# Kernel optimization log

Measured on AMD Instinct MI355X. Metric: run time of the kernel, lower is better.

Reference implementation:

```python
import jax, jax.numpy as jnp
import numpy as np

B, S, D, H, DFF = 4, 2048, 2048, 16, 8192
DH = D // H
THETA = 10000.0
EPS = 1e-5


def rmsnorm(x, g):
    return x * jax.lax.rsqrt(jnp.mean(x * x, axis=-1, keepdims=True) + EPS) * g


def rope(x, pos):
    # x: [B, H, S, DH]; rotate interleaved even/odd pairs
    half = DH // 2
    inv_freq = THETA ** (-(jnp.arange(half, dtype=jnp.float32) * 2.0) / DH)  # [half]
    ang = pos.astype(jnp.float32)[:, None] * inv_freq  # [S, half]
    cos, sin = jnp.cos(ang), jnp.sin(ang)
    x1, x2 = x[..., 0::2], x[..., 1::2]
    r1 = x1 * cos - x2 * sin
    r2 = x1 * sin + x2 * cos
    return jnp.stack([r1, r2], axis=-1).reshape(x.shape)


def setup_inputs() -> dict:
    key = jax.random.key(0)
    ks = jax.random.split(key, 12)
    s = 0.02
    return {
        "x": jax.random.normal(ks[0], (B, S, D), dtype=jnp.float32),
        "attention_mask": jnp.ones((S, S), dtype=bool),
        "wq": jax.random.normal(ks[1], (D, D), dtype=jnp.float32) * s,
        "wk": jax.random.normal(ks[2], (D, D), dtype=jnp.float32) * s,
        "wv": jax.random.normal(ks[3], (D, D), dtype=jnp.float32) * s,
        "wo": jax.random.normal(ks[4], (D, D), dtype=jnp.float32) * s,
        "w1": jax.random.normal(ks[5], (DFF, D), dtype=jnp.float32) * s,
        "w2": jax.random.normal(ks[6], (D, DFF), dtype=jnp.float32) * s,
        "w3": jax.random.normal(ks[7], (DFF, D), dtype=jnp.float32) * s,
        "g1": jnp.ones((D,), dtype=jnp.float32),
        "g2": jnp.ones((D,), dtype=jnp.float32),
    }


def reference(x, attention_mask, wq, wk, wv, wo, w1, w2, w3, g1, g2):
    pos = jnp.arange(x.shape[-2])
    # pre-norm attention
    h = rmsnorm(x, g1)
    q = (h @ wq.T).reshape(B, S, H, DH).transpose(0, 2, 1, 3)
    k = (h @ wk.T).reshape(B, S, H, DH).transpose(0, 2, 1, 3)
    v = (h @ wv.T).reshape(B, S, H, DH).transpose(0, 2, 1, 3)
    q = rope(q, pos)
    k = rope(k, pos)
    scores = jnp.einsum("bhqd,bhkd->bhqk", q, k) / np.float32(np.sqrt(DH))
    scores = jnp.where(attention_mask, scores, jnp.float32(-1e9))
    attn = jax.nn.softmax(scores, axis=-1)
    o = jnp.einsum("bhqk,bhkd->bhqd", attn, v)
    o = o.transpose(0, 2, 1, 3).reshape(B, S, D) @ wo.T
    x = x + o
    # pre-norm SwiGLU FFN
    h2 = rmsnorm(x, g2)
    ffn = (jax.nn.silu(h2 @ w1.T) * (h2 @ w3.T)) @ w2.T
    return x + ffn
```

## Files before the change

### kernel.cpp

```cpp
#include <hip/hip_runtime.h>
#include <cstdint>
#include <cstddef>

#define B_   4
#define S_   2048
#define D_   2048
#define H_   16
#define DH_  128
#define DFF_ 8192
#define LOG2E 1.4426950408889634f

typedef __bf16 bf16_t;
typedef __bf16 bf16x4 __attribute__((ext_vector_type(4)));
typedef __bf16 bf16x8 __attribute__((ext_vector_type(8)));
typedef float  f32x4  __attribute__((ext_vector_type(4)));

#define MFMA16 __builtin_amdgcn_mfma_f32_16x16x32_bf16

__device__ __forceinline__ void glds16(const void* g, void* l) {
  __builtin_amdgcn_global_load_lds((__attribute__((address_space(1))) void*)g,
                                   (__attribute__((address_space(3))) void*)l,
                                   16, 0, 0);
}

__global__ __launch_bounds__(256) void cvt_kernel(const float* __restrict__ in,
                                                  bf16_t* __restrict__ out, int n8) {
  int i = blockIdx.x * 256 + threadIdx.x;
  if (i >= n8) return;
  const float4* p4 = (const float4*)in;
  float4 a = p4[2 * (size_t)i];
  float4 b = p4[2 * (size_t)i + 1];
  bf16x8 o;
  o[0] = (bf16_t)a.x; o[1] = (bf16_t)a.y; o[2] = (bf16_t)a.z; o[3] = (bf16_t)a.w;
  o[4] = (bf16_t)b.x; o[5] = (bf16_t)b.y; o[6] = (bf16_t)b.z; o[7] = (bf16_t)b.w;
  ((bf16x8*)out)[i] = o;
}

__global__ __launch_bounds__(256) void rmsnorm_kernel(const float* __restrict__ x,
                                                      const float* __restrict__ g,
                                                      bf16_t* __restrict__ out) {
  const int row = blockIdx.x, tid = threadIdx.x;
  const float* xr = x + (size_t)row * D_;
  float4 a = ((const float4*)xr)[tid * 2];
  float4 b = ((const float4*)xr)[tid * 2 + 1];
  float ss = a.x*a.x + a.y*a.y + a.z*a.z + a.w*a.w
           + b.x*b.x + b.y*b.y + b.z*b.z + b.w*b.w;
#pragma unroll
  for (int m = 1; m < 64; m <<= 1) ss += __shfl_xor(ss, m);
  __shared__ float red[4];
  if ((tid & 63) == 0) red[tid >> 6] = ss;
  __syncthreads();
  float tot = red[0] + red[1] + red[2] + red[3];
  float rms = rsqrtf(tot * (1.0f / D_) + 1e-5f);
  float4 ga = ((const float4*)g)[tid * 2];
  float4 gb = ((const float4*)g)[tid * 2 + 1];
  bf16x8 o;
  o[0] = (bf16_t)(a.x * rms * ga.x); o[1] = (bf16_t)(a.y * rms * ga.y);
  o[2] = (bf16_t)(a.z * rms * ga.z); o[3] = (bf16_t)(a.w * rms * ga.w);
  o[4] = (bf16_t)(b.x * rms * gb.x); o[5] = (bf16_t)(b.y * rms * gb.y);
  o[6] = (bf16_t)(b.z * rms * gb.z); o[7] = (bf16_t)(b.w * rms * gb.w);
  ((bf16x8*)out)[(size_t)row * 256 + tid] = o;
}


#define Q_RD_A(d, mg)                                                         \
  do {                                                                        \
    const char* p_ = ldsb + (d) * 32768 + (wm * 128 + (mg) * 64 + l15) * 128; \
    _Pragma("unroll") for (int i_ = 0; i_ < 4; i_++) {                        \
      afr[i_][0] = *(const bf16x8*)(p_ + i_ * 2048 + acol0);                  \
      afr[i_][1] = *(const bf16x8*)(p_ + i_ * 2048 + acol1);                  \
    }                                                                         \
  } while (0)

#define Q_RD_B(dst, d, ng)                                                    \
  do {                                                                        \
    const char* p_ = ldsb + 65536 + (d) * 32768 +                             \
                     (wn * 64 + (ng) * 32 + l15) * 128;                       \
    _Pragma("unroll") for (int j_ = 0; j_ < 2; j_++) {                        \
      dst[j_][0] = *(const bf16x8*)(p_ + j_ * 2048 + acol0);                  \
      dst[j_][1] = *(const bf16x8*)(p_ + j_ * 2048 + acol1);                  \
    }                                                                         \
  } while (0)

#define Q_STAGE_A(d, kt)                                                      \
  do {                                                                        \
    char* dst_ = ldsb + (d) * 32768 + o0;                                     \
    const bf16_t* s_ = Asrc + (size_t)(kt) * 64;                              \
    glds16(s_, dst_);                                                         \
    glds16(s_ + 64 * (size_t)K, dst_ + 8192);                                 \
    glds16(s_ + 128 * (size_t)K, dst_ + 16384);                               \
    glds16(s_ + 192 * (size_t)K, dst_ + 24576);                               \
  } while (0)

#define Q_STAGE_B(d, kt)                                                      \
  do {                                                                        \
    char* dst_ = ldsb + 65536 + (d) * 32768 + o0;                             \
    const bf16_t* s_ = Wsrc + (size_t)(kt) * 64;                              \
    glds16(s_, dst_);                                                         \
    glds16(s_ + 64 * (size_t)K, dst_ + 8192);                                 \
    glds16(s_ + 128 * (size_t)K, dst_ + 16384);                               \
    glds16(s_ + 192 * (size_t)K, dst_ + 24576);                               \
  } while (0)

#define Q_MFMA(mg, ng, bsrc)                                                  \
  do {                                                                        \
    __builtin_amdgcn_s_setprio(1);                                            \
    _Pragma("unroll") for (int i_ = 0; i_ < 4; i_++)                          \
    _Pragma("unroll") for (int j_ = 0; j_ < 2; j_++) {                        \
      acc[(mg)*4 + i_][(ng)*2 + j_] =                                         \
          MFMA16(afr[i_][0], bsrc[j_][0], acc[(mg)*4 + i_][(ng)*2 + j_], 0,0,0); \
      acc[(mg)*4 + i_][(ng)*2 + j_] =                                         \
          MFMA16(afr[i_][1], bsrc[j_][1], acc[(mg)*4 + i_][(ng)*2 + j_], 0,0,0); \
    }                                                                         \
    __builtin_amdgcn_s_setprio(0);                                            \
  } while (0)

#define PHASE_FENCE()                                                         \
  do {                                                                        \
    __builtin_amdgcn_sched_barrier(0);                                        \
    __builtin_amdgcn_s_barrier();                                             \
  } while (0)

#define GEMM_EPILOGUE()                                                       \
  _Pragma("unroll") for (int m = 0; m < 8; m++) {                             \
    const int gr = m0 + wm * 128 + m * 16 + lg * 4;                           \
    _Pragma("unroll") for (int nn = 0; nn < 4; nn++) {                        \
      const int gc = n0 + wn * 64 + nn * 16 + l15;                            \
      if constexpr (EPI == 4) {                                               \
        const int seg = gc >> 11;                                             \
        const int gcl = gc & 2047;                                            \
        if (seg < 2) {                                                        \
          bf16_t* o = seg ? outb2 : outb;                                     \
          _Pragma("unroll") for (int r = 0; r < 4; r++)                       \
            o[(size_t)(gr + r) * D_ + gcl] = (bf16_t)acc[m][nn][r];           \
        } else {                                                              \
          const int bb = gr >> 11, ss = gr & 2047;                            \
          bf16x4 pk;                                                          \
          _Pragma("unroll") for (int r = 0; r < 4; r++) pk[r] = (bf16_t)acc[m][nn][r]; \
          *(bf16x4*)(outb3 + ((size_t)bb * D_ + gcl) * S_ + ss) = pk;         \
        }                                                                     \
      } else {                                                                \
        _Pragma("unroll") for (int r = 0; r < 4; r++) {                       \
          size_t idx = (size_t)(gr + r) * N + gc;                             \
          if constexpr (EPI == 0) {                                           \
            outb[idx] = (bf16_t)acc[m][nn][r];                                \
          } else if constexpr (EPI == 1) {                                    \
            outf[idx] = acc[m][nn][r] + addf[idx];                            \
          } else {                                                            \
            float a1v = (float)addb[idx];                                     \
            outb[idx] = (bf16_t)(a1v / (1.0f + expf(-a1v)) * acc[m][nn][r]);  \
          }                                                                   \
        }                                                                     \
      }                                                                       \
    }                                                                         \
  }

#define GEMM_PREAMBLE()                                                       \
  __shared__ char ldsb[131072];                                               \
  const int tid = threadIdx.x;                                                \
  const int wid = tid >> 6, l = tid & 63, l15 = l & 15, lg = l >> 4;          \
  const int wm = wid >> 2, wn = wid & 3;                                      \
  const int nwg = gridDim.x;                                                  \
  int wg = (int)blockIdx.x;                                                   \
  wg = (wg & 7) * (nwg >> 3) + (wg >> 3);                                     \
  const int ntn = N >> 8;                                                     \
  const int ntm = M >> 8;                                                     \
  const int wide = 4 * ntm;                                                   \
  const int grp = wg / wide;                                                  \
  const int rem = wg % wide;                                                  \
  const int m0 = (rem >> 2) << 8;                                             \
  const int n0 = ((grp << 2) + (rem & 3)) << 8;                               \
  f32x4 acc[8][4];                                                            \
  const f32x4 z4 = {0.f, 0.f, 0.f, 0.f};                                      \
  _Pragma("unroll") for (int i = 0; i < 8; i++)                               \
  _Pragma("unroll") for (int j = 0; j < 4; j++) acc[i][j] = z4;               \
  const int o0 = tid * 16;                                                    \
  const int srow = o0 >> 7;                                                   \
  const int ssw = ((o0 & 127) ^ ((srow & 7) << 4)) >> 1;                      \
  const bf16_t* Asrc = A + (size_t)(m0 + srow) * K + ssw;                     \
  const bf16_t* Wsrc = W + (size_t)(n0 + srow) * K + ssw;                     \
  const int rsw = (l15 & 7) << 4;                                             \
  const int acol0 = (lg * 16) ^ rsw;                                          \
  const int acol1 = (64 + lg * 16) ^ rsw;

template <int EPI>
__global__ __launch_bounds__(512, 2) void gemm256(const bf16_t* __restrict__ A,
                                                  const bf16_t* __restrict__ W,
                                                  const float* __restrict__ addf,
                                                  const bf16_t* __restrict__ addb,
                                                  bf16_t* __restrict__ outb,
                                                  bf16_t* __restrict__ outb2,
                                                  bf16_t* __restrict__ outb3,
                                                  float* __restrict__ outf,
                                                  int M, int N, int K) {
  GEMM_PREAMBLE()
  bf16x8 afr[4][2], bfr[2][2];

  const int NT = K >> 6;
  Q_STAGE_A(0, 0);
  Q_STAGE_B(0, 0);
  asm volatile("s_waitcnt vmcnt(0)" ::: "memory");
  __builtin_amdgcn_s_barrier();

  for (int t = 0; t < NT; t++) {
    const int d = t & 1;
    const bool pf = (t + 1 < NT);
    Q_RD_A(d, 0);
    Q_RD_B(bfr, d, 0);
    if (pf) Q_STAGE_A(d ^ 1, t + 1);
    PHASE_FENCE();
    Q_MFMA(0, 0, bfr);
    PHASE_FENCE();
    Q_RD_B(bfr, d, 1);
    if (pf) Q_STAGE_B(d ^ 1, t + 1);
    PHASE_FENCE();
    Q_MFMA(0, 1, bfr);
    PHASE_FENCE();
    Q_RD_A(d, 1);
    PHASE_FENCE();
    Q_MFMA(1, 1, bfr);
    PHASE_FENCE();
    Q_RD_B(bfr, d, 0);
    PHASE_FENCE();
    Q_MFMA(1, 0, bfr);
    asm volatile("s_waitcnt lgkmcnt(0) vmcnt(0)" ::: "memory");
    __builtin_amdgcn_sched_barrier(0);
    __builtin_amdgcn_s_barrier();
  }

  GEMM_EPILOGUE()
}

__global__ __launch_bounds__(256) void rope_kernel(bf16_t* __restrict__ buf) {
  size_t i = (size_t)blockIdx.x * 256 + threadIdx.x;
  int pi = (int)(i & 63);
  size_t rh = i >> 6;
  int srow = (int)((rh / H_) % S_);
  float inv = expf((float)pi * (-9.210340371976184f / 64.0f));
  float ang = (float)srow * inv;
  float c = cosf(ang), sn = sinf(ang);
  bf16_t* p = buf + i * 2;
  float x1 = (float)p[0], x2 = (float)p[1];
  p[0] = (bf16_t)(x1 * c - x2 * sn);
  p[1] = (bf16_t)(x1 * sn + x2 * c);
}

__global__ __launch_bounds__(256) void attn_kernel(const bf16_t* __restrict__ Q,
                                                   const bf16_t* __restrict__ Kb,
                                                   const bf16_t* __restrict__ Vt,
                                                   bf16_t* __restrict__ O) {
  const int qt = blockIdx.x, h = blockIdx.y, b = blockIdx.z;
  const int tid = threadIdx.x;
  const int wid = tid >> 6, l = tid & 63, l15 = l & 15, lg = l >> 4;

  __shared__ bf16_t Klds[64 * 128];
  __shared__ bf16_t Vlds[128 * 64];
  __shared__ bf16_t Plds[4][16 * 72];

  const int q0 = qt * 64 + wid * 16;
  const f32x4 z4 = {0.f, 0.f, 0.f, 0.f};

  bf16x8 qf[4];
  {
    const bf16_t* qp = Q + ((size_t)(b * S_ + q0 + l15)) * D_ + h * DH_ + lg * 8;
#pragma unroll
    for (int kk = 0; kk < 4; kk++) qf[kk] = *(const bf16x8*)(qp + kk * 32);
  }
  f32x4 of[8];
#pragma unroll
  for (int f = 0; f < 8; f++) of[f] = z4;
  float m_run = -1e30f, l_run = 0.f;

  const int o0 = tid * 16;
  const int krow0 = o0 >> 8;
  const int scol = ((o0 & 255) ^ ((krow0 & 7) << 4)) >> 1;
  const int vrow0 = o0 >> 7;
  const int vcol = ((o0 & 127) ^ ((vrow0 & 7) << 4)) >> 1;

  const size_t bh_off = ((size_t)b * S_) * D_ + (size_t)h * DH_;
  const bf16_t* vtbase = Vt + ((size_t)b * D_ + h * DH_) * S_;

  for (int kv0 = 0; kv0 < S_; kv0 += 64) {
    const bf16_t* kbase = Kb + bh_off + (size_t)kv0 * D_;
#pragma unroll
    for (int s = 0; s < 4; s++)
      glds16(kbase + (size_t)(krow0 + 16 * s) * D_ + scol,
             (char*)Klds + s * 4096 + wid * 1024);
#pragma unroll
    for (int s = 0; s < 4; s++)
      glds16(vtbase + (size_t)(vrow0 + 32 * s) * S_ + kv0 + vcol,
             (char*)Vlds + s * 4096 + wid * 1024);
    __syncthreads();

    f32x4 st[4];
#pragma unroll
    for (int c = 0; c < 4; c++) {
      st[c] = z4;
      const int row = c * 16 + l15;
      const char* kr = (const char*)Klds + row * 256;
      const int sw = (row & 7) << 4;
#pragma unroll
      for (int kk = 0; kk < 4; kk++) {
        bf16x8 kf = *(const bf16x8*)(kr + ((kk * 64 + lg * 16) ^ sw));
        st[c] = MFMA16(kf, qf[kk], st[c], 0, 0, 0);
      }
    }

    float s[16];
#pragma unroll
    for (int c = 0; c < 4; c++)
#pragma unroll
      for (int r = 0; r < 4; r++) s[c * 4 + r] = st[c][r] * 0.08838834764831845f;
    float pm = s[0];
#pragma unroll
    for (int i = 1; i < 16; i++) pm = fmaxf(pm, s[i]);
    pm = fmaxf(pm, __shfl_xor(pm, 16));
    pm = fmaxf(pm, __shfl_xor(pm, 32));
    float mnew = fmaxf(m_run, pm);
    float alpha = exp2f((m_run - mnew) * LOG2E);
    float p[16], ts = 0.f;
#pragma unroll
    for (int i = 0; i < 16; i++) { p[i] = exp2f((s[i] - mnew) * LOG2E); ts += p[i]; }
    ts += __shfl_xor(ts, 16);
    ts += __shfl_xor(ts, 32);
    l_run = l_run * alpha + ts;
    m_run = mnew;

    float aq[4];
#pragma unroll
    for (int r = 0; r < 4; r++) aq[r] = __shfl(alpha, lg * 4 + r);
#pragma unroll
    for (int f = 0; f < 8; f++)
#pragma unroll
      for (int r = 0; r < 4; r++) of[f][r] *= aq[r];

    bf16_t* pw = &Plds[wid][0];
#pragma unroll
    for (int c = 0; c < 4; c++)
#pragma unroll
      for (int r = 0; r < 4; r++)
        pw[l15 * 72 + c * 16 + lg * 4 + r] = (bf16_t)p[c * 4 + r];
    asm volatile("s_waitcnt lgkmcnt(0)" ::: "memory");
    bf16x8 pa0 = *(const bf16x8*)(pw + l15 * 72 + lg * 8);
    bf16x8 pa1 = *(const bf16x8*)(pw + l15 * 72 + 32 + lg * 8);
#pragma unroll
    for (int f = 0; f < 8; f++) {
      const int row = 16 * f + l15;
      const char* vr = (const char*)Vlds + row * 128;
      const int sw = (row & 7) << 4;
      bf16x8 bv0 = *(const bf16x8*)(vr + ((lg * 16) ^ sw));
      bf16x8 bv1 = *(const bf16x8*)(vr + ((64 + lg * 16) ^ sw));
      of[f] = MFMA16(pa0, bv0, of[f], 0, 0, 0);
      of[f] = MFMA16(pa1, bv1, of[f], 0, 0, 0);
    }
    __syncthreads();
  }

  float inv[4];
#pragma unroll
  for (int r = 0; r < 4; r++) inv[r] = 1.0f / __shfl(l_run, lg * 4 + r);
#pragma unroll
  for (int f = 0; f < 8; f++)
#pragma unroll
    for (int r = 0; r < 4; r++)
      O[((size_t)(b * S_ + q0 + lg * 4 + r)) * D_ + h * DH_ + 16 * f + l15] =
          (bf16_t)(of[f][r] * inv[r]);
}

extern "C" void kernel_launch(void* const* d_in, const int* in_sizes, int n_in,
                              void* d_out, int out_size, void* d_ws, size_t ws_size,
                              hipStream_t stream) {
  const float* x  = (const float*)d_in[0];
  const float* wq = (const float*)d_in[2];
  const float* wk = (const float*)d_in[3];
  const float* wv = (const float*)d_in[4];
  const float* wo = (const float*)d_in[5];
  const float* w1 = (const float*)d_in[6];
  const float* w2 = (const float*)d_in[7];
  const float* w3 = (const float*)d_in[8];
  const float* g1 = (const float*)d_in[9];
  const float* g2 = (const float*)d_in[10];
  float* out = (float*)d_out;

  const size_t ND = (size_t)D_ * D_;
  const size_t NF = (size_t)DFF_ * D_;
  const size_t SLOT = NF * 2;
  char* base = (char*)d_ws;
  bf16_t* wslot = (bf16_t*)(base);
  bf16_t* h1    = (bf16_t*)(base + 1 * SLOT);
  bf16_t* qb    = (bf16_t*)(base + 2 * SLOT);
  bf16_t* kb    = (bf16_t*)(base + 3 * SLOT);
  bf16_t* vt    = (bf16_t*)(base + 4 * SLOT);
  bf16_t* ob    = (bf16_t*)(base + 5 * SLOT);
  bf16_t* h2    = h1;
  bf16_t* g     = qb;
  float*  x1    = out;

  auto cvt = [&](const float* in, bf16_t* o, size_t n) {
    int n8 = (int)(n / 8);
    cvt_kernel<<<(n8 + 255) / 256, 256, 0, stream>>>(in, o, n8);
  };

  rmsnorm_kernel<<<B_ * S_, 256, 0, stream>>>(x, g1, h1);

  cvt(wq, wslot, ND);
  cvt(wk, wslot + ND, ND);
  cvt(wv, wslot + 2 * ND, ND);
  const int gqkv3 = (8192 / 256) * (6144 / 256);
  gemm256<4><<<gqkv3, 512, 0, stream>>>(h1, wslot, nullptr, nullptr,
                                        qb, kb, vt, nullptr, 8192, 6144, 2048);

  rope_kernel<<<(B_ * S_ * H_ * 64) / 256, 256, 0, stream>>>(qb);
  rope_kernel<<<(B_ * S_ * H_ * 64) / 256, 256, 0, stream>>>(kb);

  dim3 ga(S_ / 64, H_, B_);
  attn_kernel<<<ga, 256, 0, stream>>>(qb, kb, vt, ob);

  const int gqkv = (8192 / 256) * (2048 / 256);
  cvt(wo, wslot, ND);
  gemm256<1><<<gqkv, 512, 0, stream>>>(ob, wslot, x, nullptr,
                                       nullptr, nullptr, nullptr, x1, 8192, 2048, 2048);

  rmsnorm_kernel<<<B_ * S_, 256, 0, stream>>>(x1, g2, h2);

  const int gff = (8192 / 256) * (8192 / 256);
  cvt(w1, wslot, NF);
  gemm256<0><<<gff, 512, 0, stream>>>(h2, wslot, nullptr, nullptr,
                                      g, nullptr, nullptr, nullptr, 8192, 8192, 2048);

  cvt(w3, wslot, NF);
  gemm256<2><<<gff, 512, 0, stream>>>(h2, wslot, nullptr, g,
                                      g, nullptr, nullptr, nullptr, 8192, 8192, 2048);

  cvt(w2, wslot, NF);
  gemm256<1><<<gqkv, 512, 0, stream>>>(g, wslot, x1, nullptr,
                                       nullptr, nullptr, nullptr, x1, 8192, 2048, 8192);
}
```

Baseline: 1.437 ms.

## Add 128x256-tile GEMM with higher occupancy for FFN w1/w3 projections

Adds a new GEMM kernel with 128x256 output tiles, a single-buffered 48KB LDS stage and launch bounds requesting 4 blocks per CU. It replaces the 256x256 pipelined GEMM for the two 8192x8192 FFN up-projections. The aim is to raise occupancy and let multiple workgroups hide latency instead of relying on explicit software pipelining. In exchange the kernel waits on vmcnt(0) every K step with no prefetch overlap, and the smaller tile gives less reuse per loaded byte.

After: 1.436 ms. No clear change (-0.1%).

```diff
diff --git a/kernel.cpp b/kernel.cpp
--- a/kernel.cpp
+++ b/kernel.cpp
@@ -231,6 +231,100 @@
   GEMM_EPILOGUE()
 }
 
+template <int EPI>
+__global__ __launch_bounds__(512, 4) void gemm256h(const bf16_t* __restrict__ A,
+                                                   const bf16_t* __restrict__ W,
+                                                   const bf16_t* __restrict__ addb,
+                                                   bf16_t* __restrict__ outb,
+                                                   int M, int N, int K) {
+  __shared__ char ldsb[49152];
+  const int tid = threadIdx.x;
+  const int wid = tid >> 6, l = tid & 63, l15 = l & 15, lg = l >> 4;
+  const int wm = wid >> 2, wn = wid & 3;
+
+  const int nwg = gridDim.x;
+  int wg = (int)blockIdx.x;
+  wg = (wg & 7) * (nwg >> 3) + (wg >> 3);
+  const int ntm = M >> 7;
+  const int wide = 4 * ntm;
+  const int grp = wg / wide;
+  const int rem = wg % wide;
+  const int m0 = (rem >> 2) << 7;
+  const int n0 = ((grp << 2) + (rem & 3)) << 8;
+
+  f32x4 acc[4][4];
+  const f32x4 z4 = {0.f, 0.f, 0.f, 0.f};
+#pragma unroll
+  for (int i = 0; i < 4; i++)
+#pragma unroll
+    for (int j = 0; j < 4; j++) acc[i][j] = z4;
+
+  const int o0 = tid * 16;
+  const int srow = o0 >> 7;
+  const int ssw = ((o0 & 127) ^ ((srow & 7) << 4)) >> 1;
+  const bf16_t* Asrc = A + (size_t)(m0 + srow) * K + ssw;
+  const bf16_t* Wsrc = W + (size_t)(n0 + srow) * K + ssw;
+  const int rsw = (l15 & 7) << 4;
+  const int acol0 = (lg * 16) ^ rsw;
+  const int acol1 = (64 + lg * 16) ^ rsw;
+
+  const int NT = K >> 6;
+  for (int t = 0; t < NT; t++) {
+    const bf16_t* as = Asrc + (size_t)t * 64;
+    glds16(as, ldsb + o0);
+    glds16(as + 64 * (size_t)K, ldsb + 8192 + o0);
+    const bf16_t* ws = Wsrc + (size_t)t * 64;
+    glds16(ws, ldsb + 16384 + o0);
+    glds16(ws + 64 * (size_t)K, ldsb + 24576 + o0);
+    glds16(ws + 128 * (size_t)K, ldsb + 32768 + o0);
+    glds16(ws + 192 * (size_t)K, ldsb + 40960 + o0);
+    asm volatile("s_waitcnt vmcnt(0)" ::: "memory");
+    __builtin_amdgcn_s_barrier();
+    __builtin_amdgcn_sched_barrier(0);
+    bf16x8 af[4][2];
+#pragma unroll
+    for (int fi = 0; fi < 4; fi++) {
+      const char* p = ldsb + (wm * 64 + fi * 16 + l15) * 128;
+      af[fi][0] = *(const bf16x8*)(p + acol0);
+      af[fi][1] = *(const bf16x8*)(p + acol1);
+    }
+    __builtin_amdgcn_s_setprio(1);
+#pragma unroll
+    for (int n = 0; n < 4; n++) {
+      const char* p = ldsb + 16384 + (wn * 64 + n * 16 + l15) * 128;
+      bf16x8 b0 = *(const bf16x8*)(p + acol0);
+      bf16x8 b1 = *(const bf16x8*)(p + acol1);
+#pragma unroll
+      for (int m = 0; m < 4; m++) {
+        acc[m][n] = MFMA16(af[m][0], b0, acc[m][n], 0, 0, 0);
+        acc[m][n] = MFMA16(af[m][1], b1, acc[m][n], 0, 0, 0);
+      }
+    }
+    __builtin_amdgcn_s_setprio(0);
+    __builtin_amdgcn_sched_barrier(0);
+    __builtin_amdgcn_s_barrier();
+  }
+
+#pragma unroll
+  for (int m = 0; m < 4; m++) {
+    const int gr = m0 + wm * 64 + m * 16 + lg * 4;
+#pragma unroll
+    for (int n = 0; n < 4; n++) {
+      const int gc = n0 + wn * 64 + n * 16 + l15;
+#pragma unroll
+      for (int r = 0; r < 4; r++) {
+        size_t idx = (size_t)(gr + r) * N + gc;
+        if constexpr (EPI == 0) {
+          outb[idx] = (bf16_t)acc[m][n][r];
+        } else {
+          float a1v = (float)addb[idx];
+          outb[idx] = (bf16_t)(a1v / (1.0f + expf(-a1v)) * acc[m][n][r]);
+        }
+      }
+    }
+  }
+}
+
 __global__ __launch_bounds__(256) void rope_kernel(bf16_t* __restrict__ buf) {
   size_t i = (size_t)blockIdx.x * 256 + threadIdx.x;
   int pi = (int)(i & 63);
@@ -423,14 +517,12 @@
 
   rmsnorm_kernel<<<B_ * S_, 256, 0, stream>>>(x1, g2, h2);
 
-  const int gff = (8192 / 256) * (8192 / 256);
+  const int gffh = (8192 / 128) * (8192 / 256);
   cvt(w1, wslot, NF);
-  gemm256<0><<<gff, 512, 0, stream>>>(h2, wslot, nullptr, nullptr,
-                                      g, nullptr, nullptr, nullptr, 8192, 8192, 2048);
+  gemm256h<0><<<gffh, 512, 0, stream>>>(h2, wslot, nullptr, g, 8192, 8192, 2048);
 
   cvt(w3, wslot, NF);
-  gemm256<2><<<gff, 512, 0, stream>>>(h2, wslot, nullptr, g,
-                                      g, nullptr, nullptr, nullptr, 8192, 8192, 2048);
+  gemm256h<2><<<gffh, 512, 0, stream>>>(h2, wslot, g, g, 8192, 8192, 2048);
 
   cvt(w2, wslot, NF);
   gemm256<1><<<gqkv, 512, 0, stream>>>(g, wslot, x1, nullptr,
```
